# Kernel tuning notes

Hardware: AMD Instinct MI355X
Metric: run time of the kernel (lower is better)

Reference implementation:

```python
import jax, jax.numpy as jnp
import numpy as np

B, S, E, H = 2, 2048, 1024, 16
D = E // H  # head_size = 64


def setup_inputs() -> dict:
    key = jax.random.key(0)
    ks = jax.random.split(key, 11)
    sc = 0.02
    return {
        "q": jax.random.normal(ks[0], (B, S, E), jnp.float32),
        "k": jax.random.normal(ks[1], (B, S, E), jnp.float32),
        "v": jax.random.normal(ks[2], (B, S, E), jnp.float32),
        "Wq": jax.random.normal(ks[3], (E, E), jnp.float32) * sc,
        "bq": jnp.zeros((E,), jnp.float32),
        "Wk": jax.random.normal(ks[4], (E, E), jnp.float32) * sc,
        "bk": jnp.zeros((E,), jnp.float32),
        "Wv": jax.random.normal(ks[5], (E, E), jnp.float32) * sc,
        "bv": jnp.zeros((E,), jnp.float32),
        "Wo": jax.random.normal(ks[6], (E, E), jnp.float32) * sc,
        "bo": jnp.zeros((E,), jnp.float32),
    }


def reference(q, k, v, Wq, bq, Wk, bk, Wv, bv, Wo, bo):
    # torch Linear: y = x @ W.T + b
    qh = (q @ Wq.T + bq).reshape(B, S, H, D)
    kh = (k @ Wk.T + bk).reshape(B, S, H, D)
    vh = (v @ Wv.T + bv).reshape(B, S, H, D)
    # NOTE: module scales by 1/sqrt(num_heads), not 1/sqrt(head_size)
    scores = jnp.einsum('bqhe,bkhe->bhqk', qh, kh) / jnp.sqrt(jnp.float32(H))
    attn = jax.nn.softmax(scores, axis=-1)  # dropout is identity in eval
    out = jnp.einsum('bhql,blhd->bqhd', attn, vh)  # [B,S,H,D]
    out = out.reshape(B, S, E)
    return out @ Wo.T + bo
```

## Files before the change

kernel.cpp:

```cpp
#include <hip/hip_runtime.h>

typedef __bf16 bf16x8 __attribute__((ext_vector_type(8)));
typedef __bf16 bf16x4 __attribute__((ext_vector_type(4)));
typedef float  f32x4  __attribute__((ext_vector_type(4)));
typedef short  s16x4  __attribute__((ext_vector_type(4)));

#define AS1 __attribute__((address_space(1)))
#define AS3 __attribute__((address_space(3)))

__device__ inline void gload_lds16(const void* g, void* l) {
  __builtin_amdgcn_global_load_lds((AS1 void*)(g), (AS3 void*)(l), 16, 0, 0);
}

#if __has_builtin(__builtin_amdgcn_exp2f)
#define EXP2(x) __builtin_amdgcn_exp2f(x)
#else
#define EXP2(x) exp2f(x)
#endif

#if __has_builtin(__builtin_amdgcn_mfma_f32_16x16x16bf16_1k)
#define PV_K16 1
#define MFMA16(a, b, c) __builtin_amdgcn_mfma_f32_16x16x16bf16_1k(a, b, c, 0, 0, 0)
#else
#define PV_K16 0
#endif

__device__ inline short bf2s(__bf16 x) {
  union { __bf16 b; short s; } u; u.b = x; return u.s;
}

#define CB 2
#define CS 2048
#define CE 1024
#define CH 16
#define CD 64
#define GM 4096
#define GN 1024
#define GK 1024

#define QSCALE 0.36067376022224087f

#define WS_WQ  0
#define WS_WK  1048576
#define WS_WV  2097152
#define WS_WO  3145728
#define WS_XQ  4194304
#define WS_XK  8388608
#define WS_XV  12582912
#define WS_QH  16777216
#define WS_KH  20971520
#define WS_VT  25165824
#define WS_AO  WS_XQ

__global__ __launch_bounds__(256) void convert_all(
    const float* __restrict__ q, const float* __restrict__ k, const float* __restrict__ v,
    const float* __restrict__ wq, const float* __restrict__ wk,
    const float* __restrict__ wv, const float* __restrict__ wo,
    __bf16* __restrict__ ws) {
  long idx = ((long)blockIdx.x * 256 + threadIdx.x) * 8;
  const float* src;
  __bf16* dst;
  if (idx < 12582912) {
    int a = (int)(idx >> 22);
    long within = idx & 4194303;
    src = (a == 0 ? q : (a == 1 ? k : v)) + within;
    dst = ws + WS_XQ + (long)a * 4194304 + within;
  } else {
    long widx = idx - 12582912;
    int a = (int)(widx >> 20);
    long within = widx & 1048575;
    src = (a == 0 ? wq : (a == 1 ? wk : (a == 2 ? wv : wo))) + within;
    dst = ws + widx;
  }
  float4 f0 = *(const float4*)src;
  float4 f1 = *(const float4*)(src + 4);
  bf16x8 o;
  o[0] = (__bf16)f0.x; o[1] = (__bf16)f0.y; o[2] = (__bf16)f0.z; o[3] = (__bf16)f0.w;
  o[4] = (__bf16)f1.x; o[5] = (__bf16)f1.y; o[6] = (__bf16)f1.z; o[7] = (__bf16)f1.w;
  *(bf16x8*)dst = o;
}

#define GEMM_BK64_BODY(A_PTR, B_PTR, KLEN)                                          \
  __shared__ __bf16 As[8192];                                                       \
  __shared__ __bf16 Bs[8192];                                                       \
  const int tid = threadIdx.x;                                                      \
  const int w = tid >> 6, l = tid & 63;                                             \
  const int wm = w >> 1, wn = w & 1;                                                \
  const int bm = blockIdx.y * 128, bn = blockIdx.x * 128;                           \
  const int lr = l & 15, lq = l >> 4;                                               \
  f32x4 acc[4][4] = {};                                                             \
  const int srow = w * 8 + (l >> 3);                                                \
  const int scol = ((l & 7) ^ ((l >> 3) & 7)) * 8;                                  \
  const __bf16* ga0 = (A_PTR) + (size_t)(bm + srow) * GK + scol;                    \
  const __bf16* gb0 = (B_PTR) + (size_t)(bn + srow) * GK + scol;                    \
  const int dstg = w * 64 + l;                                                      \
  for (int k0 = 0; k0 < (KLEN); k0 += 64) {                                         \
    __syncthreads();                                                                \
    for (int i = 0; i < 4; i++) {                                                   \
      gload_lds16(ga0 + (size_t)(i * 32) * GK + k0, &As[(i * 256 + dstg) * 8]);     \
      gload_lds16(gb0 + (size_t)(i * 32) * GK + k0, &Bs[(i * 256 + dstg) * 8]);     \
    }                                                                               \
    __syncthreads();                                                                \
    for (int kk = 0; kk < 2; kk++) {                                                \
      bf16x8 af[4], bfr[4];                                                         \
      for (int mi = 0; mi < 4; mi++) {                                              \
        const int row = wm * 64 + mi * 16 + lr;                                     \
        af[mi] = *(const bf16x8*)&As[(row * 8 + ((kk * 4 + lq) ^ (row & 7))) * 8];  \
      }                                                                             \
      for (int ni = 0; ni < 4; ni++) {                                              \
        const int row = wn * 64 + ni * 16 + lr;                                     \
        bfr[ni] = *(const bf16x8*)&Bs[(row * 8 + ((kk * 4 + lq) ^ (row & 7))) * 8]; \
      }                                                                             \
      for (int mi = 0; mi < 4; mi++)                                                \
        for (int ni = 0; ni < 4; ni++)                                              \
          acc[mi][ni] = __builtin_amdgcn_mfma_f32_16x16x32_bf16(af[mi], bfr[ni],    \
                                                                acc[mi][ni], 0, 0, 0); \
    }                                                                               \
  }

__global__ __launch_bounds__(256) void qkv_gemm(
    const __bf16* __restrict__ Xq, const __bf16* __restrict__ Xk, const __bf16* __restrict__ Xv,
    const __bf16* __restrict__ Wq, const __bf16* __restrict__ Wk, const __bf16* __restrict__ Wv,
    const float* __restrict__ bq, const float* __restrict__ bk, const float* __restrict__ bv,
    __bf16* __restrict__ Qh, __bf16* __restrict__ Kh, __bf16* __restrict__ Vt) {
  const int mode = blockIdx.z;
  const __bf16* A  = mode == 0 ? Xq : (mode == 1 ? Xk : Xv);
  const __bf16* Bw = mode == 0 ? Wq : (mode == 1 ? Wk : Wv);
  const float* bias = mode == 0 ? bq : (mode == 1 ? bk : bv);

  GEMM_BK64_BODY(A, Bw, GK)

  const int row0 = bm + wm * 64;
  const int col0 = bn + wn * 64;
  for (int ni = 0; ni < 4; ni++) {
    const int col = col0 + ni * 16 + lr;
    const float bb = bias[col];
    for (int mi = 0; mi < 4; mi++) {
      const int row = row0 + mi * 16 + lq * 4;
      if (mode == 0) {
        for (int r = 0; r < 4; r++)
          Qh[(size_t)(row + r) * GN + col] = (__bf16)((acc[mi][ni][r] + bb) * QSCALE);
      } else if (mode == 1) {
        for (int r = 0; r < 4; r++)
          Kh[(size_t)(row + r) * GN + col] = (__bf16)(acc[mi][ni][r] + bb);
      } else {
        const int b = row >> 11, s = row & 2047;
        const int h = col >> 6, d = col & 63;
        bf16x4 pk;
        for (int r = 0; r < 4; r++) pk[r] = (__bf16)(acc[mi][ni][r] + bb);
        *(bf16x4*)&Vt[(size_t)((b * CH + h) * CD + d) * CS + s] = pk;
      }
    }
  }
}

__global__ __launch_bounds__(256) void gemm_wo(const __bf16* __restrict__ Ain,
                                               const __bf16* __restrict__ Bw,
                                               const float* __restrict__ bias,
                                               float* __restrict__ O) {
  GEMM_BK64_BODY(Ain, Bw, GK)

  const int row0 = bm + wm * 64;
  const int col0 = bn + wn * 64;
  for (int ni = 0; ni < 4; ni++) {
    const int col = col0 + ni * 16 + lr;
    const float bb = bias[col];
    for (int mi = 0; mi < 4; mi++) {
      const int row = row0 + mi * 16 + lq * 4;
      for (int r = 0; r < 4; r++)
        O[(size_t)(row + r) * GN + col] = acc[mi][ni][r] + bb;
    }
  }
}

__global__ __launch_bounds__(256, 2) void attn(const __bf16* __restrict__ Qh,
                                               const __bf16* __restrict__ Kh,
                                               const __bf16* __restrict__ Vt,
                                               __bf16* __restrict__ AO) {
  __shared__ __bf16 Ks[8192];
  __shared__ __bf16 Vs[8192];

  const int tid = threadIdx.x, w = tid >> 6, l = tid & 63;
  const int lr = l & 15, lq = l >> 4;
  const int bh = blockIdx.x;
  const int b = bh >> 4, h = bh & 15;
  const int q0 = blockIdx.y * 128 + w * 32;

  bf16x8 qf[2][2];
  for (int mi = 0; mi < 2; mi++)
    for (int kk = 0; kk < 2; kk++)
      qf[mi][kk] = *(const bf16x8*)&Qh[((size_t)b * CS + q0 + mi * 16 + lr) * CE + h * CD + kk * 32 + lq * 8];

  f32x4 o[2][4] = {};
  float lsum[2] = {0.f, 0.f};
#if !PV_K16
  const bool hi_half = (lq & 1);
#endif

  for (int kt = 0; kt < CS / 128; kt++) {
    __syncthreads();
    for (int i = 0; i < 4; i++) {
      const int j = w * 2 + (i >> 1), hf = i & 1;
      const int key = (hf * 64 + l) ^ ((j & 3) * 2);
      gload_lds16(&Kh[((size_t)b * CS + kt * 128 + key) * CE + h * CD + j * 8],
                  &Ks[(j * 128 + hf * 64) * 8]);
    }
    for (int i = 0; i < 4; i++) {
      const int j2 = w * 4 + i;
      const int d = l ^ ((j2 & 1) * 4);
      gload_lds16(&Vt[((size_t)bh * CD + d) * CS + kt * 128 + j2 * 8],
                  &Vs[(j2 * 64) * 8]);
    }
    __syncthreads();

    f32x4 sa[2][8] = {};
    for (int kk = 0; kk < 2; kk++) {
      bf16x8 kf[8];
      for (int ni = 0; ni < 8; ni++)
        kf[ni] = *(const bf16x8*)&Ks[((kk * 4 + lq) * 128 + ((ni * 16 + lr) ^ (lq * 2))) * 8];
      for (int mi = 0; mi < 2; mi++)
        for (int ni = 0; ni < 8; ni++)
          sa[mi][ni] = __builtin_amdgcn_mfma_f32_16x16x32_bf16(kf[ni], qf[mi][kk], sa[mi][ni], 0, 0, 0);
    }

#if PV_K16
    for (int ni = 0; ni < 8; ni++) {
      s16x4 pa4[2];
      for (int mi = 0; mi < 2; mi++)
        for (int r = 0; r < 4; r++) {
          const float p = EXP2(sa[mi][ni][r]);
          lsum[mi] += p;
          pa4[mi][r] = bf2s((__bf16)p);
        }
      const int j2 = ni * 2 + (lq >> 1);
      const int base = j2 * 64;
      const int sw = (j2 & 1) * 4;
      for (int di = 0; di < 4; di++) {
        const int dslot = (di * 16 + lr) ^ sw;
        const s16x4 vb4 = *(const s16x4*)&Vs[(base + dslot) * 8 + (lq & 1) * 4];
        for (int mi = 0; mi < 2; mi++)
          o[mi][di] = MFMA16(pa4[mi], vb4, o[mi][di]);
      }
    }
#else
    for (int ni = 0; ni < 8; ni++) {
      bf16x8 pa[2];
      for (int mi = 0; mi < 2; mi++) {
        bf16x8 f;
        for (int r = 0; r < 4; r++) {
          const float p = EXP2(sa[mi][ni][r]);
          lsum[mi] += p;
          const __bf16 bv = (__bf16)p;
          f[r]     = hi_half ? (__bf16)0.f : bv;
          f[4 + r] = hi_half ? bv : (__bf16)0.f;
        }
        pa[mi] = f;
      }
      for (int di = 0; di < 4; di++) {
        const bf16x8 vb = *(const bf16x8*)&Vs[((ni * 2 + (lq >> 1)) * 64 + ((di * 16 + lr) ^ ((lq >> 1) * 4))) * 8];
        for (int mi = 0; mi < 2; mi++)
          o[mi][di] = __builtin_amdgcn_mfma_f32_16x16x32_bf16(pa[mi], vb, o[mi][di], 0, 0, 0);
      }
    }
#endif
  }

  for (int mi = 0; mi < 2; mi++) {
    lsum[mi] += __shfl_xor(lsum[mi], 16, 64);
    lsum[mi] += __shfl_xor(lsum[mi], 32, 64);
  }

  for (int mi = 0; mi < 2; mi++) {
    f32x4 rv;
    for (int r = 0; r < 4; r++) rv[r] = 1.0f / __shfl(lsum[mi], lq * 4 + r, 64);
    for (int di = 0; di < 4; di++)
      for (int r = 0; r < 4; r++) {
        const size_t s = q0 + mi * 16 + lq * 4 + r;
        AO[((size_t)b * CS + s) * CE + h * CD + di * 16 + lr] = (__bf16)(o[mi][di][r] * rv[r]);
      }
  }
}

extern "C" void kernel_launch(void* const* d_in, const int* in_sizes, int n_in,
                              void* d_out, int out_size, void* d_ws, size_t ws_size,
                              hipStream_t stream) {
  (void)in_sizes; (void)n_in; (void)out_size; (void)ws_size;
  const float* q  = (const float*)d_in[0];
  const float* k  = (const float*)d_in[1];
  const float* v  = (const float*)d_in[2];
  const float* Wq = (const float*)d_in[3];
  const float* bq = (const float*)d_in[4];
  const float* Wk = (const float*)d_in[5];
  const float* bk = (const float*)d_in[6];
  const float* Wv = (const float*)d_in[7];
  const float* bv = (const float*)d_in[8];
  const float* Wo = (const float*)d_in[9];
  const float* bo = (const float*)d_in[10];

  __bf16* ws = (__bf16*)d_ws;
  __bf16 *Wq_b = ws + WS_WQ, *Wk_b = ws + WS_WK, *Wv_b = ws + WS_WV, *Wo_b = ws + WS_WO;
  __bf16 *Xq = ws + WS_XQ, *Xk = ws + WS_XK, *Xv = ws + WS_XV;
  __bf16 *Qh = ws + WS_QH, *Kh = ws + WS_KH, *Vt = ws + WS_VT;
  __bf16 *AO = ws + WS_AO;

  convert_all<<<8192, 256, 0, stream>>>(q, k, v, Wq, Wk, Wv, Wo, ws);

  qkv_gemm<<<dim3(GN / 128, GM / 128, 3), 256, 0, stream>>>(
      Xq, Xk, Xv, Wq_b, Wk_b, Wv_b, bq, bk, bv, Qh, Kh, Vt);

  attn<<<dim3(CB * CH, CS / 128), 256, 0, stream>>>(Qh, Kh, Vt, AO);

  gemm_wo<<<dim3(GN / 128, GM / 128), 256, 0, stream>>>(AO, Wo_b, bo, (float*)d_out);
}
```

Before: 229.3 us.

## Double-buffer K/V tiles in attention with async LDS prefetch and MFMA priority

The attention kernel now keeps two LDS buffers for the K and V tiles and issues global-to-LDS loads for the next tile before computing on the current one, so memory latency overlaps with MFMA work. Address computation is hoisted out of the loop into per-thread base pointers, and one waitcnt plus barrier per iteration replaces the two syncthreads. s_setprio is raised around the MFMA sections to favour matrix issue. LDS use doubles to 64KB per block, which may limit occupancy with launch bounds of 2 blocks per CU.

Result: slower. 235.0 us (+2.5%).

```diff
diff --git a/kernel.cpp b/kernel.cpp
--- a/kernel.cpp
+++ b/kernel.cpp
@@ -177,8 +177,8 @@
                                                const __bf16* __restrict__ Kh,
                                                const __bf16* __restrict__ Vt,
                                                __bf16* __restrict__ AO) {
-  __shared__ __bf16 Ks[8192];
-  __shared__ __bf16 Vs[8192];
+  __shared__ __bf16 Ks[2][8192];
+  __shared__ __bf16 Vs[2][8192];
 
   const int tid = threadIdx.x, w = tid >> 6, l = tid & 63;
   const int lr = l & 15, lq = l >> 4;
@@ -191,37 +191,53 @@
     for (int kk = 0; kk < 2; kk++)
       qf[mi][kk] = *(const bf16x8*)&Qh[((size_t)b * CS + q0 + mi * 16 + lr) * CE + h * CD + kk * 32 + lq * 8];
 
+  const __bf16* ksrc[4]; const __bf16* vsrc[4];
+  int koff[4], voff[4];
+  for (int i = 0; i < 4; i++) {
+    const int j = w * 2 + (i >> 1), hf = i & 1;
+    const int key = (hf * 64 + l) ^ ((j & 3) * 2);
+    ksrc[i] = &Kh[((size_t)b * CS + key) * CE + h * CD + j * 8];
+    koff[i] = (j * 128 + hf * 64) * 8;
+    const int j2 = w * 4 + i;
+    const int d = l ^ ((j2 & 1) * 4);
+    vsrc[i] = &Vt[((size_t)bh * CD + d) * CS + j2 * 8];
+    voff[i] = (j2 * 64) * 8;
+  }
+
   f32x4 o[2][4] = {};
   float lsum[2] = {0.f, 0.f};
 #if !PV_K16
   const bool hi_half = (lq & 1);
 #endif
 
+  for (int i = 0; i < 4; i++) gload_lds16(ksrc[i], &Ks[0][koff[i]]);
+  for (int i = 0; i < 4; i++) gload_lds16(vsrc[i], &Vs[0][voff[i]]);
+  asm volatile("s_waitcnt vmcnt(0)" ::: "memory");
+  __builtin_amdgcn_s_barrier();
+
   for (int kt = 0; kt < CS / 128; kt++) {
-    __syncthreads();
-    for (int i = 0; i < 4; i++) {
-      const int j = w * 2 + (i >> 1), hf = i & 1;
-      const int key = (hf * 64 + l) ^ ((j & 3) * 2);
-      gload_lds16(&Kh[((size_t)b * CS + kt * 128 + key) * CE + h * CD + j * 8],
-                  &Ks[(j * 128 + hf * 64) * 8]);
-    }
-    for (int i = 0; i < 4; i++) {
-      const int j2 = w * 4 + i;
-      const int d = l ^ ((j2 & 1) * 4);
-      gload_lds16(&Vt[((size_t)bh * CD + d) * CS + kt * 128 + j2 * 8],
-                  &Vs[(j2 * 64) * 8]);
-    }
-    __syncthreads();
+    const int cur = kt & 1;
+    const __bf16* kb = Ks[cur];
+    const __bf16* vb = Vs[cur];
+
+    if (kt + 1 < CS / 128) {
+      for (int i = 0; i < 4; i++)
+        gload_lds16(ksrc[i] + (size_t)(kt + 1) * (128 * CE), &Ks[cur ^ 1][koff[i]]);
+      for (int i = 0; i < 4; i++)
+        gload_lds16(vsrc[i] + (kt + 1) * 128, &Vs[cur ^ 1][voff[i]]);
+    }
 
     f32x4 sa[2][8] = {};
+    __builtin_amdgcn_s_setprio(1);
     for (int kk = 0; kk < 2; kk++) {
       bf16x8 kf[8];
       for (int ni = 0; ni < 8; ni++)
-        kf[ni] = *(const bf16x8*)&Ks[((kk * 4 + lq) * 128 + ((ni * 16 + lr) ^ (lq * 2))) * 8];
+        kf[ni] = *(const bf16x8*)&kb[((kk * 4 + lq) * 128 + ((ni * 16 + lr) ^ (lq * 2))) * 8];
       for (int mi = 0; mi < 2; mi++)
         for (int ni = 0; ni < 8; ni++)
           sa[mi][ni] = __builtin_amdgcn_mfma_f32_16x16x32_bf16(kf[ni], qf[mi][kk], sa[mi][ni], 0, 0, 0);
     }
+    __builtin_amdgcn_s_setprio(0);
 
 #if PV_K16
     for (int ni = 0; ni < 8; ni++) {
@@ -235,12 +251,14 @@
       const int j2 = ni * 2 + (lq >> 1);
       const int base = j2 * 64;
       const int sw = (j2 & 1) * 4;
+      __builtin_amdgcn_s_setprio(1);
       for (int di = 0; di < 4; di++) {
         const int dslot = (di * 16 + lr) ^ sw;
-        const s16x4 vb4 = *(const s16x4*)&Vs[(base + dslot) * 8 + (lq & 1) * 4];
+        const s16x4 vb4 = *(const s16x4*)&vb[(base + dslot) * 8 + (lq & 1) * 4];
         for (int mi = 0; mi < 2; mi++)
           o[mi][di] = MFMA16(pa4[mi], vb4, o[mi][di]);
       }
+      __builtin_amdgcn_s_setprio(0);
     }
 #else
     for (int ni = 0; ni < 8; ni++) {
@@ -250,19 +268,22 @@
         for (int r = 0; r < 4; r++) {
           const float p = EXP2(sa[mi][ni][r]);
           lsum[mi] += p;
-          const __bf16 bv = (__bf16)p;
-          f[r]     = hi_half ? (__bf16)0.f : bv;
-          f[4 + r] = hi_half ? bv : (__bf16)0.f;
+          const __bf16 bv2 = (__bf16)p;
+          f[r]     = hi_half ? (__bf16)0.f : bv2;
+          f[4 + r] = hi_half ? bv2 : (__bf16)0.f;
         }
         pa[mi] = f;
       }
       for (int di = 0; di < 4; di++) {
-        const bf16x8 vb = *(const bf16x8*)&Vs[((ni * 2 + (lq >> 1)) * 64 + ((di * 16 + lr) ^ ((lq >> 1) * 4))) * 8];
+        const bf16x8 vbf = *(const bf16x8*)&vb[((ni * 2 + (lq >> 1)) * 64 + ((di * 16 + lr) ^ ((lq >> 1) * 4))) * 8];
         for (int mi = 0; mi < 2; mi++)
-          o[mi][di] = __builtin_amdgcn_mfma_f32_16x16x32_bf16(pa[mi], vb, o[mi][di], 0, 0, 0);
+          o[mi][di] = __builtin_amdgcn_mfma_f32_16x16x32_bf16(pa[mi], vbf, o[mi][di], 0, 0, 0);
       }
     }
 #endif
+
+    asm volatile("s_waitcnt vmcnt(0)" ::: "memory");
+    __builtin_amdgcn_s_barrier();
   }
 
   for (int mi = 0; mi < 2; mi++) {
```

## Halve attention query tile per block and remap GEMM blocks across XCDs

Applied to the files above, without the earlier changes.

The attention kernel now has each wave handle 16 query rows instead of 32, so each block covers 64 queries. The grid doubles to 1024 blocks and launch bounds allow 4 blocks per CU, which is meant to raise occupancy and cut register pressure. The cost is that K/V tiles are loaded from global into LDS twice as often per query. Separately, the GEMM block index is permuted so consecutive tiles land on the same XCD, aiming for better L2 reuse on MI355X's chiplet layout.

Measured after the change: 255.3 us. 1.11x slower.

```diff
diff --git a/kernel.cpp b/kernel.cpp
--- a/kernel.cpp
+++ b/kernel.cpp
@@ -86,7 +86,10 @@
   const int tid = threadIdx.x;                                                      \
   const int w = tid >> 6, l = tid & 63;                                             \
   const int wm = w >> 1, wn = w & 1;                                                \
-  const int bm = blockIdx.y * 128, bn = blockIdx.x * 128;                           \
+  const int orig = blockIdx.y * gridDim.x + blockIdx.x;                             \
+  const int cpx = (gridDim.x * gridDim.y) >> 3;                                     \
+  const int wgid = (orig & 7) * cpx + (orig >> 3);                                  \
+  const int bm = (wgid / gridDim.x) * 128, bn = (wgid % gridDim.x) * 128;           \
   const int lr = l & 15, lq = l >> 4;                                               \
   f32x4 acc[4][4] = {};                                                             \
   const int srow = w * 8 + (l >> 3);                                                \
@@ -173,7 +176,7 @@
   }
 }
 
-__global__ __launch_bounds__(256, 2) void attn(const __bf16* __restrict__ Qh,
+__global__ __launch_bounds__(256, 4) void attn(const __bf16* __restrict__ Qh,
                                                const __bf16* __restrict__ Kh,
                                                const __bf16* __restrict__ Vt,
                                                __bf16* __restrict__ AO) {
@@ -184,15 +187,14 @@
   const int lr = l & 15, lq = l >> 4;
   const int bh = blockIdx.x;
   const int b = bh >> 4, h = bh & 15;
-  const int q0 = blockIdx.y * 128 + w * 32;
-
-  bf16x8 qf[2][2];
-  for (int mi = 0; mi < 2; mi++)
-    for (int kk = 0; kk < 2; kk++)
-      qf[mi][kk] = *(const bf16x8*)&Qh[((size_t)b * CS + q0 + mi * 16 + lr) * CE + h * CD + kk * 32 + lq * 8];
-
-  f32x4 o[2][4] = {};
-  float lsum[2] = {0.f, 0.f};
+  const int q0 = blockIdx.y * 64 + w * 16;
+
+  bf16x8 qf[2];
+  for (int kk = 0; kk < 2; kk++)
+    qf[kk] = *(const bf16x8*)&Qh[((size_t)b * CS + q0 + lr) * CE + h * CD + kk * 32 + lq * 8];
+
+  f32x4 o[4] = {};
+  float lsum = 0.f;
 #if !PV_K16
   const bool hi_half = (lq & 1);
 #endif
@@ -213,72 +215,64 @@
     }
     __syncthreads();
 
-    f32x4 sa[2][8] = {};
+    f32x4 sa[8] = {};
     for (int kk = 0; kk < 2; kk++) {
       bf16x8 kf[8];
       for (int ni = 0; ni < 8; ni++)
         kf[ni] = *(const bf16x8*)&Ks[((kk * 4 + lq) * 128 + ((ni * 16 + lr) ^ (lq * 2))) * 8];
-      for (int mi = 0; mi < 2; mi++)
-        for (int ni = 0; ni < 8; ni++)
-          sa[mi][ni] = __builtin_amdgcn_mfma_f32_16x16x32_bf16(kf[ni], qf[mi][kk], sa[mi][ni], 0, 0, 0);
+      for (int ni = 0; ni < 8; ni++)
+        sa[ni] = __builtin_amdgcn_mfma_f32_16x16x32_bf16(kf[ni], qf[kk], sa[ni], 0, 0, 0);
     }
 
 #if PV_K16
     for (int ni = 0; ni < 8; ni++) {
-      s16x4 pa4[2];
-      for (int mi = 0; mi < 2; mi++)
-        for (int r = 0; r < 4; r++) {
-          const float p = EXP2(sa[mi][ni][r]);
-          lsum[mi] += p;
-          pa4[mi][r] = bf2s((__bf16)p);
-        }
+      s16x4 pa4;
+      for (int r = 0; r < 4; r++) {
+        const float p = EXP2(sa[ni][r]);
+        lsum += p;
+        pa4[r] = bf2s((__bf16)p);
+      }
       const int j2 = ni * 2 + (lq >> 1);
       const int base = j2 * 64;
       const int sw = (j2 & 1) * 4;
       for (int di = 0; di < 4; di++) {
         const int dslot = (di * 16 + lr) ^ sw;
         const s16x4 vb4 = *(const s16x4*)&Vs[(base + dslot) * 8 + (lq & 1) * 4];
-        for (int mi = 0; mi < 2; mi++)
-          o[mi][di] = MFMA16(pa4[mi], vb4, o[mi][di]);
+        o[di] = MFMA16(pa4, vb4, o[di]);
       }
     }
 #else
     for (int ni = 0; ni < 8; ni++) {
-      bf16x8 pa[2];
-      for (int mi = 0; mi < 2; mi++) {
+      bf16x8 pa;
+      {
         bf16x8 f;
         for (int r = 0; r < 4; r++) {
-          const float p = EXP2(sa[mi][ni][r]);
-          lsum[mi] += p;
-          const __bf16 bv = (__bf16)p;
-          f[r]     = hi_half ? (__bf16)0.f : bv;
-          f[4 + r] = hi_half ? bv : (__bf16)0.f;
+          const float p = EXP2(sa[ni][r]);
+          lsum += p;
+          const __bf16 bv2 = (__bf16)p;
+          f[r]     = hi_half ? (__bf16)0.f : bv2;
+          f[4 + r] = hi_half ? bv2 : (__bf16)0.f;
         }
-        pa[mi] = f;
+        pa = f;
       }
       for (int di = 0; di < 4; di++) {
-        const bf16x8 vb = *(const bf16x8*)&Vs[((ni * 2 + (lq >> 1)) * 64 + ((di * 16 + lr) ^ ((lq >> 1) * 4))) * 8];
-        for (int mi = 0; mi < 2; mi++)
-          o[mi][di] = __builtin_amdgcn_mfma_f32_16x16x32_bf16(pa[mi], vb, o[mi][di], 0, 0, 0);
+        const bf16x8 vbf = *(const bf16x8*)&Vs[((ni * 2 + (lq >> 1)) * 64 + ((di * 16 + lr) ^ ((lq >> 1) * 4))) * 8];
+        o[di] = __builtin_amdgcn_mfma_f32_16x16x32_bf16(pa, vbf, o[di], 0, 0, 0);
       }
     }
 #endif
   }
 
-  for (int mi = 0; mi < 2; mi++) {
-    lsum[mi] += __shfl_xor(lsum[mi], 16, 64);
-    lsum[mi] += __shfl_xor(lsum[mi], 32, 64);
-  }
-
-  for (int mi = 0; mi < 2; mi++) {
-    f32x4 rv;
-    for (int r = 0; r < 4; r++) rv[r] = 1.0f / __shfl(lsum[mi], lq * 4 + r, 64);
-    for (int di = 0; di < 4; di++)
-      for (int r = 0; r < 4; r++) {
-        const size_t s = q0 + mi * 16 + lq * 4 + r;
-        AO[((size_t)b * CS + s) * CE + h * CD + di * 16 + lr] = (__bf16)(o[mi][di][r] * rv[r]);
-      }
-  }
+  lsum += __shfl_xor(lsum, 16, 64);
+  lsum += __shfl_xor(lsum, 32, 64);
+
+  f32x4 rv;
+  for (int r = 0; r < 4; r++) rv[r] = 1.0f / __shfl(lsum, lq * 4 + r, 64);
+  for (int di = 0; di < 4; di++)
+    for (int r = 0; r < 4; r++) {
+      const size_t s = q0 + lq * 4 + r;
+      AO[((size_t)b * CS + s) * CE + h * CD + di * 16 + lr] = (__bf16)(o[di][r] * rv[r]);
+    }
 }
 
 extern "C" void kernel_launch(void* const* d_in, const int* in_sizes, int n_in,
@@ -308,7 +302,7 @@
   qkv_gemm<<<dim3(GN / 128, GM / 128, 3), 256, 0, stream>>>(
       Xq, Xk, Xv, Wq_b, Wk_b, Wv_b, bq, bk, bv, Qh, Kh, Vt);
 
-  attn<<<dim3(CB * CH, CS / 128), 256, 0, stream>>>(Qh, Kh, Vt, AO);
+  attn<<<dim3(CB * CH, CS / 64), 256, 0, stream>>>(Qh, Kh, Vt, AO);
 
   gemm_wo<<<dim3(GN / 128, GM / 128), 256, 0, stream>>>(AO, Wo_b, bo, (float*)d_out);
 }
```

## Load two key tiles per barrier in attention and remap GEMM blocks across XCDs

Applied to the files above, without the earlier changes.

The attention kernel now loads two 128-key K/V chunks into doubled LDS buffers per iteration. This halves the number of barrier pairs and gives more outstanding global loads per sync. The GEMM macro also remaps block IDs so that consecutive tiles land on the same XCD, aiming for better L2 locality. The doubled LDS (64KB per block) may reduce occupancy below the launch-bounds target of 2 blocks per CU, and the remap assumes the grid size is divisible by 8.

New measurement: 317.0 us. 38.2% more time.

```diff
diff --git a/kernel.cpp b/kernel.cpp
--- a/kernel.cpp
+++ b/kernel.cpp
@@ -86,7 +86,10 @@
   const int tid = threadIdx.x;                                                      \
   const int w = tid >> 6, l = tid & 63;                                             \
   const int wm = w >> 1, wn = w & 1;                                                \
-  const int bm = blockIdx.y * 128, bn = blockIdx.x * 128;                           \
+  const int orig = blockIdx.y * gridDim.x + blockIdx.x;                             \
+  const int cpx = (gridDim.x * gridDim.y) >> 3;                                     \
+  const int wgid = (orig & 7) * cpx + (orig >> 3);                                  \
+  const int bm = (wgid / gridDim.x) * 128, bn = (wgid % gridDim.x) * 128;           \
   const int lr = l & 15, lq = l >> 4;                                               \
   f32x4 acc[4][4] = {};                                                             \
   const int srow = w * 8 + (l >> 3);                                                \
@@ -177,8 +180,8 @@
                                                const __bf16* __restrict__ Kh,
                                                const __bf16* __restrict__ Vt,
                                                __bf16* __restrict__ AO) {
-  __shared__ __bf16 Ks[8192];
-  __shared__ __bf16 Vs[8192];
+  __shared__ __bf16 Ks[2][8192];
+  __shared__ __bf16 Vs[2][8192];
 
   const int tid = threadIdx.x, w = tid >> 6, l = tid & 63;
   const int lr = l & 15, lq = l >> 4;
@@ -197,72 +200,77 @@
   const bool hi_half = (lq & 1);
 #endif
 
-  for (int kt = 0; kt < CS / 128; kt++) {
+  for (int kt = 0; kt < CS / 256; kt++) {
     __syncthreads();
-    for (int i = 0; i < 4; i++) {
-      const int j = w * 2 + (i >> 1), hf = i & 1;
-      const int key = (hf * 64 + l) ^ ((j & 3) * 2);
-      gload_lds16(&Kh[((size_t)b * CS + kt * 128 + key) * CE + h * CD + j * 8],
-                  &Ks[(j * 128 + hf * 64) * 8]);
-    }
-    for (int i = 0; i < 4; i++) {
-      const int j2 = w * 4 + i;
-      const int d = l ^ ((j2 & 1) * 4);
-      gload_lds16(&Vt[((size_t)bh * CD + d) * CS + kt * 128 + j2 * 8],
-                  &Vs[(j2 * 64) * 8]);
+    for (int c = 0; c < 2; c++) {
+      const int keybase = kt * 256 + c * 128;
+      for (int i = 0; i < 4; i++) {
+        const int j = w * 2 + (i >> 1), hf = i & 1;
+        const int key = (hf * 64 + l) ^ ((j & 3) * 2);
+        gload_lds16(&Kh[((size_t)b * CS + keybase + key) * CE + h * CD + j * 8],
+                    &Ks[c][(j * 128 + hf * 64) * 8]);
+      }
+      for (int i = 0; i < 4; i++) {
+        const int j2 = w * 4 + i;
+        const int d = l ^ ((j2 & 1) * 4);
+        gload_lds16(&Vt[((size_t)bh * CD + d) * CS + keybase + j2 * 8],
+                    &Vs[c][(j2 * 64) * 8]);
+      }
     }
     __syncthreads();
 
-    f32x4 sa[2][8] = {};
-    for (int kk = 0; kk < 2; kk++) {
-      bf16x8 kf[8];
-      for (int ni = 0; ni < 8; ni++)
-        kf[ni] = *(const bf16x8*)&Ks[((kk * 4 + lq) * 128 + ((ni * 16 + lr) ^ (lq * 2))) * 8];
-      for (int mi = 0; mi < 2; mi++)
+    for (int c = 0; c < 2; c++) {
+      f32x4 sa[2][8] = {};
+      for (int kk = 0; kk < 2; kk++) {
+        bf16x8 kf[8];
         for (int ni = 0; ni < 8; ni++)
-          sa[mi][ni] = __builtin_amdgcn_mfma_f32_16x16x32_bf16(kf[ni], qf[mi][kk], sa[mi][ni], 0, 0, 0);
+          kf[ni] = *(const bf16x8*)&Ks[c][((kk * 4 + lq) * 128 + ((ni * 16 + lr) ^ (lq * 2))) * 8];
+        for (int mi = 0; mi < 2; mi++)
+          for (int ni = 0; ni < 8; ni++)
+            sa[mi][ni] = __builtin_amdgcn_mfma_f32_16x16x32_bf16(kf[ni], qf[mi][kk], sa[mi][ni], 0, 0, 0);
+      }
+
+#if PV_K16
+      for (int ni = 0; ni < 8; ni++) {
+        s16x4 pa4[2];
+        for (int mi = 0; mi < 2; mi++)
+          for (int r = 0; r < 4; r++) {
+            const float p = EXP2(sa[mi][ni][r]);
+            lsum[mi] += p;
+            pa4[mi][r] = bf2s((__bf16)p);
+          }
+        const int j2 = ni * 2 + (lq >> 1);
+        const int base = j2 * 64;
+        const int sw = (j2 & 1) * 4;
+        for (int di = 0; di < 4; di++) {
+          const int dslot = (di * 16 + lr) ^ sw;
+          const s16x4 vb4 = *(const s16x4*)&Vs[c][(base + dslot) * 8 + (lq & 1) * 4];
+          for (int mi = 0; mi < 2; mi++)
+            o[mi][di] = MFMA16(pa4[mi], vb4, o[mi][di]);
+        }
+      }
+#else
+      for (int ni = 0; ni < 8; ni++) {
+        bf16x8 pa[2];
+        for (int mi = 0; mi < 2; mi++) {
+          bf16x8 f;
+          for (int r = 0; r < 4; r++) {
+            const float p = EXP2(sa[mi][ni][r]);
+            lsum[mi] += p;
+            const __bf16 bv2 = (__bf16)p;
+            f[r]     = hi_half ? (__bf16)0.f : bv2;
+            f[4 + r] = hi_half ? bv2 : (__bf16)0.f;
+          }
+          pa[mi] = f;
+        }
+        for (int di = 0; di < 4; di++) {
+          const bf16x8 vbf = *(const bf16x8*)&Vs[c][((ni * 2 + (lq >> 1)) * 64 + ((di * 16 + lr) ^ ((lq >> 1) * 4))) * 8];
+          for (int mi = 0; mi < 2; mi++)
+            o[mi][di] = __builtin_amdgcn_mfma_f32_16x16x32_bf16(pa[mi], vbf, o[mi][di], 0, 0, 0);
+        }
+      }
+#endif
     }
-
-#if PV_K16
-    for (int ni = 0; ni < 8; ni++) {
-      s16x4 pa4[2];
-      for (int mi = 0; mi < 2; mi++)
-        for (int r = 0; r < 4; r++) {
-          const float p = EXP2(sa[mi][ni][r]);
-          lsum[mi] += p;
-          pa4[mi][r] = bf2s((__bf16)p);
-        }
-      const int j2 = ni * 2 + (lq >> 1);
-      const int base = j2 * 64;
-      const int sw = (j2 & 1) * 4;
-      for (int di = 0; di < 4; di++) {
-        const int dslot = (di * 16 + lr) ^ sw;
-        const s16x4 vb4 = *(const s16x4*)&Vs[(base + dslot) * 8 + (lq & 1) * 4];
-        for (int mi = 0; mi < 2; mi++)
-          o[mi][di] = MFMA16(pa4[mi], vb4, o[mi][di]);
-      }
-    }
-#else
-    for (int ni = 0; ni < 8; ni++) {
-      bf16x8 pa[2];
-      for (int mi = 0; mi < 2; mi++) {
-        bf16x8 f;
-        for (int r = 0; r < 4; r++) {
-          const float p = EXP2(sa[mi][ni][r]);
-          lsum[mi] += p;
-          const __bf16 bv = (__bf16)p;
-          f[r]     = hi_half ? (__bf16)0.f : bv;
-          f[4 + r] = hi_half ? bv : (__bf16)0.f;
-        }
-        pa[mi] = f;
-      }
-      for (int di = 0; di < 4; di++) {
-        const bf16x8 vb = *(const bf16x8*)&Vs[((ni * 2 + (lq >> 1)) * 64 + ((di * 16 + lr) ^ ((lq >> 1) * 4))) * 8];
-        for (int mi = 0; mi < 2; mi++)
-          o[mi][di] = __builtin_amdgcn_mfma_f32_16x16x32_bf16(pa[mi], vb, o[mi][di], 0, 0, 0);
-      }
-    }
-#endif
   }
 
   for (int mi = 0; mi < 2; mi++) {
```
